# Performance work log

Hardware: AMD Instinct MI355X
Metric: run time of the kernel (lower is better)

## Reference

```python
import jax, jax.numpy as jnp
import numpy as np

B, S, D, H, FF = 16, 1024, 1024, 8, 4096
DH = D // H
EPS = 1e-5

def _ln(x, g, b):
    mu = jnp.mean(x, axis=-1, keepdims=True)
    var = jnp.mean((x - mu) ** 2, axis=-1, keepdims=True)
    return (x - mu) * jax.lax.rsqrt(var + EPS) * g + b

def setup_inputs() -> dict:
    key = jax.random.key(0)
    ks = jax.random.split(key, 12)
    sd = D ** -0.5
    return {
        "x": jax.random.normal(ks[0], (B, S, D), jnp.float32),
        "bias": jax.random.normal(ks[1], (S, S), jnp.float32),
        "Wq": jax.random.normal(ks[2], (D, D), jnp.float32) * sd,
        "bq": jnp.zeros((D,), jnp.float32),
        "Wk": jax.random.normal(ks[3], (D, D), jnp.float32) * sd,
        "bk": jnp.zeros((D,), jnp.float32),
        "Wv": jax.random.normal(ks[4], (D, D), jnp.float32) * sd,
        "bv": jnp.zeros((D,), jnp.float32),
        "Wo": jax.random.normal(ks[5], (D, D), jnp.float32) * sd,
        "bo": jnp.zeros((D,), jnp.float32),
        "ln1_g": jnp.ones((D,), jnp.float32),
        "ln1_b": jnp.zeros((D,), jnp.float32),
        "W1": jax.random.normal(ks[6], (FF, D), jnp.float32) * sd,
        "b1": jnp.zeros((FF,), jnp.float32),
        "W2": jax.random.normal(ks[7], (D, FF), jnp.float32) * (FF ** -0.5),
        "b2": jnp.zeros((D,), jnp.float32),
        "ln2_g": jnp.ones((D,), jnp.float32),
        "ln2_b": jnp.zeros((D,), jnp.float32),
    }

def reference(x, bias, Wq, bq, Wk, bk, Wv, bv, Wo, bo, ln1_g, ln1_b,
              W1, b1, W2, b2, ln2_g, ln2_b):
    # torch nn.Linear: y = x @ W.T + b
    Q = x @ Wq.T + bq  # [B,S,D]
    K = x @ Wk.T + bk
    V = x @ Wv.T + bv
    # Faithful to torch: plain row-major reshape [B,S,H*dh] -> [B*H,S,dh]
    Q = Q.reshape(B * H, S, DH)
    K = K.reshape(B * H, S, DH)
    V = V.reshape(B * H, S, DH)
    scale = DH ** -0.5
    scores = jnp.einsum('bqd,bkd->bqk', Q, K)  # [B*H,S,S]
    scores = (scores + bias[None]) * scale      # bias added BEFORE scaling, as in source
    attn = jax.nn.softmax(scores, axis=-1)
    selfattention = attn[0]
    ctx = jnp.einsum('bqk,bkd->bqd', attn, V).reshape(B, S, D)
    out = ctx @ Wo.T + bo
    out = _ln(out + x, ln1_g, ln1_b)
    # FFN
    h = jax.nn.relu(out @ W1.T + b1)
    ff = h @ W2.T + b2
    out2 = _ln(ff + out, ln2_g, ln2_b)
    return out2, selfattention
```

## Files before the change

### kernel.cpp

```cpp
#include <hip/hip_runtime.h>
#include <hip/hip_bf16.h>
#include <math.h>

typedef __attribute__((ext_vector_type(4))) float f32x4;
typedef __attribute__((ext_vector_type(8))) __bf16 bf16x8;
typedef __attribute__((ext_vector_type(4))) __bf16 bf16x4;

static constexpr float SCALE = 0.08838834764831845f;
static constexpr float SCALE_LOG2E = 0.1275174482f;

__device__ __forceinline__ void load_lds16(const void* g, void* l) {
  __builtin_amdgcn_global_load_lds(
      (const __attribute__((address_space(1))) void*)g,
      (__attribute__((address_space(3))) void*)l, 16, 0, 0);
}

__global__ __launch_bounds__(256) void cast_kernel(const float* __restrict__ s,
                                                   __bf16* __restrict__ d, int n4) {
  int i = blockIdx.x * blockDim.x + threadIdx.x;
  int stride = gridDim.x * blockDim.x;
  for (; i < n4; i += stride) {
    float4 v = reinterpret_cast<const float4*>(s)[i];
    bf16x4 o;
    o[0] = (__bf16)v.x; o[1] = (__bf16)v.y; o[2] = (__bf16)v.z; o[3] = (__bf16)v.w;
    reinterpret_cast<bf16x4*>(d)[i] = o;
  }
}

__global__ __launch_bounds__(256) void cast_weights(
    const float* __restrict__ wq, const float* __restrict__ wk,
    const float* __restrict__ wv, const float* __restrict__ wo,
    const float* __restrict__ w1, const float* __restrict__ w2,
    __bf16* __restrict__ dq, __bf16* __restrict__ dk,
    __bf16* __restrict__ dv, __bf16* __restrict__ dwo,
    __bf16* __restrict__ d1, __bf16* __restrict__ d2) {
  int i = blockIdx.x * blockDim.x + threadIdx.x;
  int stride = gridDim.x * blockDim.x;
  for (; i < 3145728; i += stride) {
    const float* s; __bf16* d; int j;
    if (i < 262144)       { s = wq; d = dq;  j = i; }
    else if (i < 524288)  { s = wk; d = dk;  j = i - 262144; }
    else if (i < 786432)  { s = wv; d = dv;  j = i - 524288; }
    else if (i < 1048576) { s = wo; d = dwo; j = i - 786432; }
    else if (i < 2097152) { s = w1; d = d1;  j = i - 1048576; }
    else                  { s = w2; d = d2;  j = i - 2097152; }
    float4 v = reinterpret_cast<const float4*>(s)[j];
    bf16x4 o;
    o[0] = (__bf16)v.x; o[1] = (__bf16)v.y; o[2] = (__bf16)v.z; o[3] = (__bf16)v.w;
    reinterpret_cast<bf16x4*>(d)[j] = o;
  }
}

__global__ __launch_bounds__(256) void scale_cast_kernel(const float* __restrict__ s,
                                                         __bf16* __restrict__ d, int n4) {
  int i = blockIdx.x * blockDim.x + threadIdx.x;
  int stride = gridDim.x * blockDim.x;
  for (; i < n4; i += stride) {
    float4 v = reinterpret_cast<const float4*>(s)[i];
    bf16x4 o;
    o[0] = (__bf16)(v.x * SCALE_LOG2E); o[1] = (__bf16)(v.y * SCALE_LOG2E);
    o[2] = (__bf16)(v.z * SCALE_LOG2E); o[3] = (__bf16)(v.w * SCALE_LOG2E);
    reinterpret_cast<bf16x4*>(d)[i] = o;
  }
}

template <int EPI>
__global__ __launch_bounds__(512, 2) void gemm_bt(
    const __bf16* __restrict__ A, const __bf16* __restrict__ Bw,
    const float* __restrict__ bvec, __bf16* __restrict__ Cb,
    float* __restrict__ Cf, int M, int N, int K) {
  __shared__ __align__(16) char sm[131072];

  const int ntn = N >> 8;
  const int nwg = gridDim.x;
  const int bid = blockIdx.x;
  const int b = (bid & 7) * (nwg >> 3) + (bid >> 3);
  const int tm = b / ntn, tn = b % ntn;
  const int t = threadIdx.x, lane = t & 63;
  const int w = t >> 6;
  const int wm = w >> 2, wn = w & 3;
  const int l15 = lane & 15, lq = lane >> 4;

  f32x4 acc[8][4] = {};

  const int r0 = t >> 3;
  const int r1 = r0 + 64;
  const int kb0 = (((t & 7) << 4) ^ ((r0 & 7) << 4));
  const int wbase = w << 10;

  auto stage = [&](int kt, int p) {
    char* base = sm + (p << 16);
    const size_t kofs = (size_t)(kb0 >> 1) + ((size_t)kt << 6);
#pragma unroll
    for (int h = 0; h < 2; ++h) {
      const __bf16* gA = A + (size_t)((tm << 8) + (h << 7) + r0) * K + kofs;
      const __bf16* gA2 = A + (size_t)((tm << 8) + (h << 7) + r1) * K + kofs;
      char* lA = base + (h << 14) + wbase;
      load_lds16(gA, lA);
      load_lds16(gA2, lA + 8192);
      const __bf16* gB = Bw + (size_t)((tn << 8) + (h << 7) + r0) * K + kofs;
      const __bf16* gB2 = Bw + (size_t)((tn << 8) + (h << 7) + r1) * K + kofs;
      char* lB = base + 32768 + (h << 14) + wbase;
      load_lds16(gB, lB);
      load_lds16(gB2, lB + 8192);
    }
  };

  stage(0, 0);
  __syncthreads();

  const int NT = K >> 6;
  const int rbB = (wn & 1) << 6;
  for (int kt = 0; kt < NT; ++kt) {
    const int p = kt & 1;
    const char* Ab = sm + (p << 16) + (wm << 14);
    const char* Bb = sm + (p << 16) + 32768 + ((wn >> 1) << 14);
    if (kt + 1 < NT) stage(kt + 1, p ^ 1);

    bf16x8 bfv[4][2];
#pragma unroll
    for (int nf = 0; nf < 4; ++nf) {
      const int r = rbB + (nf << 4) + l15;
      const int sw = (r & 7) << 4;
#pragma unroll
      for (int ks = 0; ks < 2; ++ks) {
        const int lb = (ks << 6) + (lq << 4);
        bfv[nf][ks] = *(const bf16x8*)(Bb + r * 128 + (lb ^ sw));
      }
    }
#pragma unroll
    for (int q = 0; q < 4; ++q) {
      bf16x8 af[2][2];
#pragma unroll
      for (int dm = 0; dm < 2; ++dm) {
        const int r = (((q << 1) + dm) << 4) + l15;
        const int sw = (r & 7) << 4;
#pragma unroll
        for (int ks = 0; ks < 2; ++ks) {
          const int lb = (ks << 6) + (lq << 4);
          af[dm][ks] = *(const bf16x8*)(Ab + r * 128 + (lb ^ sw));
        }
      }
#pragma unroll
      for (int ks = 0; ks < 2; ++ks)
#pragma unroll
        for (int dm = 0; dm < 2; ++dm)
#pragma unroll
          for (int nf = 0; nf < 4; ++nf)
            acc[(q << 1) + dm][nf] = __builtin_amdgcn_mfma_f32_16x16x32_bf16(
                af[dm][ks], bfv[nf][ks], acc[(q << 1) + dm][nf], 0, 0, 0);
    }
    __syncthreads();
  }

  const int row0 = (tm << 8) + (wm << 7) + (lq << 2);
  const int col0 = (tn << 8) + (wn << 6) + l15;
#pragma unroll
  for (int nf = 0; nf < 4; ++nf) {
    const int col = col0 + (nf << 4);
    const float bv = bvec[col];
#pragma unroll
    for (int mf = 0; mf < 8; ++mf) {
#pragma unroll
      for (int r = 0; r < 4; ++r) {
        const int row = row0 + (mf << 4) + r;
        float v = acc[mf][nf][r] + bv;
        if (EPI == 1) v = fmaxf(v, 0.f);
        if (EPI == 2) {
          Cf[(size_t)row * N + col] = v;
        } else if (EPI == 3) {
          size_t vt = ((size_t)(row >> 7) << 17) + ((size_t)(col & 127) << 10) +
                      ((row & 127) << 3) + (col >> 7);
          Cb[vt] = (__bf16)v;
        } else {
          Cb[(size_t)row * N + col] = (__bf16)v;
        }
      }
    }
  }
}

__global__ __launch_bounds__(512, 2) void gemm_qkv(
    const __bf16* __restrict__ A,
    const __bf16* __restrict__ Wq, const __bf16* __restrict__ Wk,
    const __bf16* __restrict__ Wv,
    const float* __restrict__ bqv, const float* __restrict__ bkv,
    const float* __restrict__ bvv,
    __bf16* __restrict__ Qo, __bf16* __restrict__ Ko, __bf16* __restrict__ VTo) {
  __shared__ __align__(16) char sm[131072];
  const int K = 1024, N = 1024;

  const int bid = blockIdx.x;
  const int b = (bid & 7) * 96 + (bid >> 3);
  const int tm = b / 12;
  const int tnt = b % 12;
  const int mi = tnt >> 2, tn = tnt & 3;
  const __bf16* Bw = (mi == 0) ? Wq : (mi == 1) ? Wk : Wv;
  const float* bvec = (mi == 0) ? bqv : (mi == 1) ? bkv : bvv;
  __bf16* Cb = (mi == 0) ? Qo : (mi == 1) ? Ko : VTo;

  const int t = threadIdx.x, lane = t & 63;
  const int w = t >> 6;
  const int wm = w >> 2, wn = w & 3;
  const int l15 = lane & 15, lq = lane >> 4;

  f32x4 acc[8][4] = {};

  const int r0 = t >> 3;
  const int r1 = r0 + 64;
  const int kb0 = (((t & 7) << 4) ^ ((r0 & 7) << 4));
  const int wbase = w << 10;

  auto stage = [&](int kt, int p) {
    char* base = sm + (p << 16);
    const size_t kofs = (size_t)(kb0 >> 1) + ((size_t)kt << 6);
#pragma unroll
    for (int h = 0; h < 2; ++h) {
      const __bf16* gA = A + (size_t)((tm << 8) + (h << 7) + r0) * K + kofs;
      const __bf16* gA2 = A + (size_t)((tm << 8) + (h << 7) + r1) * K + kofs;
      char* lA = base + (h << 14) + wbase;
      load_lds16(gA, lA);
      load_lds16(gA2, lA + 8192);
      const __bf16* gB = Bw + (size_t)((tn << 8) + (h << 7) + r0) * K + kofs;
      const __bf16* gB2 = Bw + (size_t)((tn << 8) + (h << 7) + r1) * K + kofs;
      char* lB = base + 32768 + (h << 14) + wbase;
      load_lds16(gB, lB);
      load_lds16(gB2, lB + 8192);
    }
  };

  stage(0, 0);
  __syncthreads();

  const int NT = K >> 6;
  const int rbB = (wn & 1) << 6;
  for (int kt = 0; kt < NT; ++kt) {
    const int p = kt & 1;
    const char* Ab = sm + (p << 16) + (wm << 14);
    const char* Bb = sm + (p << 16) + 32768 + ((wn >> 1) << 14);
    if (kt + 1 < NT) stage(kt + 1, p ^ 1);

    bf16x8 bfv[4][2];
#pragma unroll
    for (int nf = 0; nf < 4; ++nf) {
      const int r = rbB + (nf << 4) + l15;
      const int sw = (r & 7) << 4;
#pragma unroll
      for (int ks = 0; ks < 2; ++ks) {
        const int lb = (ks << 6) + (lq << 4);
        bfv[nf][ks] = *(const bf16x8*)(Bb + r * 128 + (lb ^ sw));
      }
    }
#pragma unroll
    for (int q = 0; q < 4; ++q) {
      bf16x8 af[2][2];
#pragma unroll
      for (int dm = 0; dm < 2; ++dm) {
        const int r = (((q << 1) + dm) << 4) + l15;
        const int sw = (r & 7) << 4;
#pragma unroll
        for (int ks = 0; ks < 2; ++ks) {
          const int lb = (ks << 6) + (lq << 4);
          af[dm][ks] = *(const bf16x8*)(Ab + r * 128 + (lb ^ sw));
        }
      }
#pragma unroll
      for (int ks = 0; ks < 2; ++ks)
#pragma unroll
        for (int dm = 0; dm < 2; ++dm)
#pragma unroll
          for (int nf = 0; nf < 4; ++nf)
            acc[(q << 1) + dm][nf] = __builtin_amdgcn_mfma_f32_16x16x32_bf16(
                af[dm][ks], bfv[nf][ks], acc[(q << 1) + dm][nf], 0, 0, 0);
    }
    __syncthreads();
  }

  const int row0 = (tm << 8) + (wm << 7) + (lq << 2);
  const int col0 = (tn << 8) + (wn << 6) + l15;
#pragma unroll
  for (int nf = 0; nf < 4; ++nf) {
    const int col = col0 + (nf << 4);
    const float bv = bvec[col];
#pragma unroll
    for (int mf = 0; mf < 8; ++mf) {
#pragma unroll
      for (int r = 0; r < 4; ++r) {
        const int row = row0 + (mf << 4) + r;
        float v = acc[mf][nf][r] + bv;
        if (mi == 2) {
          size_t vt = ((size_t)(row >> 7) << 17) + ((size_t)(col & 127) << 10) +
                      ((row & 127) << 3) + (col >> 7);
          Cb[vt] = (__bf16)v;
        } else {
          Cb[(size_t)row * N + col] = (__bf16)v;
        }
      }
    }
  }
}

__global__ __launch_bounds__(256) void attn_flash(
    const __bf16* __restrict__ Q, const __bf16* __restrict__ K,
    const __bf16* __restrict__ VT, const __bf16* __restrict__ biasS,
    __bf16* __restrict__ ctx) {
  __shared__ __bf16 Ks[64 * 128];
  __shared__ __bf16 VTs[128 * 64];
  __shared__ __bf16 Ps[4][16 * 64];

  const int bid = blockIdx.x;
  const int b = ((bid & 7) << 8) | (bid >> 3);
  const int g = b >> 4;
  const int q0 = (b & 15) << 6;
  const size_t goff = (size_t)g << 17;
  const __bf16* Qg = Q + goff;
  const __bf16* Kg = K + goff;
  const __bf16* VTg = VT + goff;

  const int t = threadIdx.x, w = t >> 6, lane = t & 63;
  const int l15 = lane & 15, lq = lane >> 4;
  const int qg = q0 + (w << 4) + l15;

  bf16x8 qf[4];
  {
    const __bf16* qrow = Qg + (size_t)qg * 128 + (lq << 3);
#pragma unroll
    for (int ec = 0; ec < 4; ++ec) qf[ec] = *(const bf16x8*)(qrow + (ec << 5));
  }
  const __bf16* bSr = biasS + ((size_t)qg << 10) + (lq << 2);

  float lrun = 0.f;
  f32x4 cacc[8] = {};

  for (int kb = 0; kb < 1024; kb += 64) {
    {
      int srow = lane >> 4;
      int sbo = (lane & 15) << 4;
#pragma unroll
      for (int i = 0; i < 4; ++i) {
        int c = (w << 2) + i;
        int r = (c << 2) + srow;
        int ke = (sbo ^ ((r & 7) << 4)) >> 1;
        load_lds16(Kg + (size_t)(kb + r) * 128 + ke, (char*)Ks + (c << 10));
      }
    }
    {
      int srow = lane >> 3;
      int sbo = (lane & 7) << 4;
#pragma unroll
      for (int i = 0; i < 4; ++i) {
        int c = (w << 2) + i;
        int e = (c << 3) + srow;
        int ke = kb + ((sbo ^ ((e & 7) << 4)) >> 1);
        load_lds16(VTg + (size_t)e * 1024 + ke, (char*)VTs + (c << 10));
      }
    }
    __syncthreads();

    f32x4 sacc[4] = {};
    __builtin_amdgcn_s_setprio(1);
#pragma unroll
    for (int ec = 0; ec < 4; ++ec) {
      const int lb = (ec << 6) + (lq << 4);
#pragma unroll
      for (int kn = 0; kn < 4; ++kn) {
        int rb = (kn << 4) + l15;
        bf16x8 kf = *(const bf16x8*)((const char*)Ks + rb * 256 + (lb ^ ((rb & 7) << 4)));
        sacc[kn] = __builtin_amdgcn_mfma_f32_16x16x32_bf16(kf, qf[ec], sacc[kn], 0, 0, 0);
      }
    }
    __builtin_amdgcn_s_setprio(0);

    const __bf16* bt = bSr + kb;
#pragma unroll
    for (int kn = 0; kn < 4; ++kn) {
      bf16x4 bb = *(const bf16x4*)(bt + (kn << 4));
      bf16x4 pk;
#pragma unroll
      for (int r = 0; r < 4; ++r) {
        float p = exp2f(fmaf(sacc[kn][r], SCALE_LOG2E, (float)bb[r]));
        lrun += p;
        pk[r] = (__bf16)p;
      }
      int bo = (kn << 5) + (lq << 3);
      *(bf16x4*)((char*)Ps[w] + l15 * 128 + (bo ^ ((l15 & 7) << 4))) = pk;
    }
    asm volatile("s_waitcnt lgkmcnt(0)" ::: "memory");
    __builtin_amdgcn_sched_barrier(0);

    __builtin_amdgcn_s_setprio(1);
#pragma unroll
    for (int ks = 0; ks < 2; ++ks) {
      const int lb = (ks << 6) + (lq << 4);
      bf16x8 paf = *(const bf16x8*)((const char*)Ps[w] + l15 * 128 + (lb ^ ((l15 & 7) << 4)));
#pragma unroll
      for (int et = 0; et < 8; ++et) {
        int e = (et << 4) + l15;
        bf16x8 vf = *(const bf16x8*)((const char*)VTs + e * 128 + (lb ^ ((e & 7) << 4)));
        cacc[et] = __builtin_amdgcn_mfma_f32_16x16x32_bf16(paf, vf, cacc[et], 0, 0, 0);
      }
    }
    __builtin_amdgcn_s_setprio(0);
    __syncthreads();
  }

  lrun += __shfl_xor(lrun, 16);
  lrun += __shfl_xor(lrun, 32);
  float lrunR[4];
#pragma unroll
  for (int r = 0; r < 4; ++r)
    lrunR[r] = __shfl(lrun, (lane & 48) + ((lane & 48) >> 2) + r);
  __bf16* cg = ctx + goff;
  const int qr = q0 + (w << 4) + (lq << 2);
#pragma unroll
  for (int et = 0; et < 8; ++et)
#pragma unroll
    for (int r = 0; r < 4; ++r) {
      float v = cacc[et][r] / lrunR[r];
      cg[(size_t)(qr + r) * 128 + (et << 4) + l15] = (__bf16)v;
    }
}

__global__ __launch_bounds__(256) void attn_head0(
    const __bf16* __restrict__ Q, const __bf16* __restrict__ K,
    const float* __restrict__ bias, float* __restrict__ out) {
  __shared__ float qrow[128];
  __shared__ float red[8];
  const int q = blockIdx.x, t = threadIdx.x;
  if (t < 128) qrow[t] = (float)Q[(size_t)q * 128 + t];
  __syncthreads();
  float s[4];
#pragma unroll
  for (int c = 0; c < 4; ++c) {
    int kc = (c << 8) + t;
    const __bf16* kr = K + (size_t)kc * 128;
    float dot = 0.f;
#pragma unroll
    for (int e = 0; e < 128; e += 8) {
      bf16x8 kv = *(const bf16x8*)(kr + e);
#pragma unroll
      for (int j = 0; j < 8; ++j) dot += qrow[e + j] * (float)kv[j];
    }
    s[c] = (dot + bias[(size_t)q * 1024 + kc]) * SCALE;
  }
  float mx = fmaxf(fmaxf(s[0], s[1]), fmaxf(s[2], s[3]));
#pragma unroll
  for (int d = 32; d >= 1; d >>= 1) mx = fmaxf(mx, __shfl_xor(mx, d));
  const int w = t >> 6, lane = t & 63;
  if (lane == 0) red[w] = mx;
  __syncthreads();
  mx = fmaxf(fmaxf(red[0], red[1]), fmaxf(red[2], red[3]));
  float ex[4], sum = 0.f;
#pragma unroll
  for (int c = 0; c < 4; ++c) { ex[c] = __expf(s[c] - mx); sum += ex[c]; }
#pragma unroll
  for (int d = 32; d >= 1; d >>= 1) sum += __shfl_xor(sum, d);
  __syncthreads();
  if (lane == 0) red[4 + w] = sum;
  __syncthreads();
  sum = red[4] + red[5] + red[6] + red[7];
  float inv = 1.f / sum;
#pragma unroll
  for (int c = 0; c < 4; ++c) out[(size_t)q * 1024 + (c << 8) + t] = ex[c] * inv;
}

template <int A_BF16, int B_BF16>
__global__ __launch_bounds__(256) void ln_res(
    const void* __restrict__ aptr, const void* __restrict__ bptr,
    const float* __restrict__ gam, const float* __restrict__ bet,
    float* __restrict__ outf, __bf16* __restrict__ outb) {
  __shared__ float red[8];
  const int row = blockIdx.x, t = threadIdx.x;
  const size_t base = (size_t)row << 10;
  float a0, a1, a2, a3;
  if (A_BF16) {
    bf16x4 va = reinterpret_cast<const bf16x4*>((const __bf16*)aptr + base)[t];
    a0 = (float)va[0]; a1 = (float)va[1]; a2 = (float)va[2]; a3 = (float)va[3];
  } else {
    float4 va = reinterpret_cast<const float4*>((const float*)aptr + base)[t];
    a0 = va.x; a1 = va.y; a2 = va.z; a3 = va.w;
  }
  float b0, b1, b2, b3;
  if (B_BF16) {
    bf16x4 vb = reinterpret_cast<const bf16x4*>((const __bf16*)bptr + base)[t];
    b0 = (float)vb[0]; b1 = (float)vb[1]; b2 = (float)vb[2]; b3 = (float)vb[3];
  } else {
    float4 vb = reinterpret_cast<const float4*>((const float*)bptr + base)[t];
    b0 = vb.x; b1 = vb.y; b2 = vb.z; b3 = vb.w;
  }
  float v0 = a0 + b0, v1 = a1 + b1, v2 = a2 + b2, v3 = a3 + b3;
  float s = v0 + v1 + v2 + v3;
  float qq = v0 * v0 + v1 * v1 + v2 * v2 + v3 * v3;
#pragma unroll
  for (int d = 32; d >= 1; d >>= 1) {
    s += __shfl_xor(s, d);
    qq += __shfl_xor(qq, d);
  }
  const int w = t >> 6, lane = t & 63;
  if (lane == 0) { red[w] = s; red[4 + w] = qq; }
  __syncthreads();
  s = red[0] + red[1] + red[2] + red[3];
  qq = red[4] + red[5] + red[6] + red[7];
  const float mu = s * (1.f / 1024.f);
  const float var = qq * (1.f / 1024.f) - mu * mu;
  const float rs = rsqrtf(var + 1e-5f);
  float4 g4 = reinterpret_cast<const float4*>(gam)[t];
  float4 b4 = reinterpret_cast<const float4*>(bet)[t];
  float o0 = (v0 - mu) * rs * g4.x + b4.x;
  float o1 = (v1 - mu) * rs * g4.y + b4.y;
  float o2 = (v2 - mu) * rs * g4.z + b4.z;
  float o3 = (v3 - mu) * rs * g4.w + b4.w;
  if (outf) reinterpret_cast<float4*>(outf + base)[t] = make_float4(o0, o1, o2, o3);
  if (outb) {
    bf16x4 ob;
    ob[0] = (__bf16)o0; ob[1] = (__bf16)o1; ob[2] = (__bf16)o2; ob[3] = (__bf16)o3;
    reinterpret_cast<bf16x4*>(outb + base)[t] = ob;
  }
}

extern "C" void kernel_launch(void* const* d_in, const int* in_sizes, int n_in,
                              void* d_out, int out_size, void* d_ws, size_t ws_size,
                              hipStream_t stream) {
  (void)in_sizes; (void)n_in; (void)out_size; (void)ws_size;
  const float* x    = (const float*)d_in[0];
  const float* bias = (const float*)d_in[1];
  const float* Wq   = (const float*)d_in[2];
  const float* bq   = (const float*)d_in[3];
  const float* Wk   = (const float*)d_in[4];
  const float* bk   = (const float*)d_in[5];
  const float* Wv   = (const float*)d_in[6];
  const float* bv   = (const float*)d_in[7];
  const float* Wo   = (const float*)d_in[8];
  const float* bo   = (const float*)d_in[9];
  const float* g1   = (const float*)d_in[10];
  const float* b1l  = (const float*)d_in[11];
  const float* W1   = (const float*)d_in[12];
  const float* b1f  = (const float*)d_in[13];
  const float* W2   = (const float*)d_in[14];
  const float* b2f  = (const float*)d_in[15];
  const float* g2   = (const float*)d_in[16];
  const float* b2l  = (const float*)d_in[17];

  char* ws = (char*)d_ws;
  size_t off = 0;
  auto alloc = [&](size_t bytes) {
    char* p = ws + off;
    off += (bytes + 255) & ~(size_t)255;
    return p;
  };
  __bf16* wqb  = (__bf16*)alloc(2097152);
  __bf16* wkb  = (__bf16*)alloc(2097152);
  __bf16* wvb  = (__bf16*)alloc(2097152);
  __bf16* wob  = (__bf16*)alloc(2097152);
  __bf16* w1b  = (__bf16*)alloc(8388608);
  __bf16* w2b  = (__bf16*)alloc(8388608);
  __bf16* biasS = (__bf16*)alloc(2097152);
  __bf16* xb   = (__bf16*)alloc(33554432);
  __bf16* Qb   = (__bf16*)alloc(4ull * 33554432);
  __bf16* Kb   = Qb + 16777216;
  __bf16* VTb  = Kb + 16777216;
  __bf16* ctxb = VTb + 16777216;
  __bf16* hb   = Qb;
  __bf16* res1b = xb;
  __bf16* attn_out_b = Qb;

  float* out2     = (float*)d_out;
  float* selfattn = (float*)d_out + 16777216;
  float* ff       = out2;

  cast_kernel<<<2048, 256, 0, stream>>>(x, xb, 16777216 / 4);
  cast_weights<<<2048, 256, 0, stream>>>(Wq, Wk, Wv, Wo, W1, W2,
                                         wqb, wkb, wvb, wob, w1b, w2b);
  scale_cast_kernel<<<512, 256, 0, stream>>>(bias, biasS, 1048576 / 4);

  gemm_qkv<<<768, 512, 0, stream>>>(xb, wqb, wkb, wvb, bq, bk, bv, Qb, Kb, VTb);

  attn_head0<<<1024, 256, 0, stream>>>(Qb, Kb, bias, selfattn);
  attn_flash<<<128 * 16, 256, 0, stream>>>(Qb, Kb, VTb, biasS, ctxb);

  gemm_bt<0><<<64 * 4, 512, 0, stream>>>(ctxb, wob, bo, attn_out_b, nullptr, 16384, 1024, 1024);

  ln_res<1, 0><<<16384, 256, 0, stream>>>(attn_out_b, x, g1, b1l, nullptr, res1b);

  gemm_bt<1><<<64 * 16, 512, 0, stream>>>(res1b, w1b, b1f, hb, nullptr, 16384, 4096, 1024);
  gemm_bt<2><<<64 * 4, 512, 0, stream>>>(hb, w2b, b2f, nullptr, ff, 16384, 1024, 4096);

  ln_res<0, 1><<<16384, 256, 0, stream>>>(ff, res1b, g2, b2l, out2, nullptr);
}
```

Baseline: 747.8 us.

## Add phased-barrier FFN GEMM, widen attention blocks, split QKV GEMM

Adds a templated GEMM (gemm_ph) for the two FFN GEMMs. It issues the next tile's global-to-LDS load after the first sub-step and uses raw s_barrier/waitcnt plus setprio around each MFMA group, so copies overlap compute with finer sync. The fused QKV GEMM is replaced by three gemm_bt launches, the V launch using the transposed epilogue. The flash attention kernel now runs 8 waves per block over 128 query rows, so each staged K/V tile is reused by twice as many rows. The first LayerNorm reads the bf16 copy of x as its residual instead of fp32, which cuts traffic but lowers residual precision.

```diff
diff --git a/kernel.cpp b/kernel.cpp
--- a/kernel.cpp
+++ b/kernel.cpp
@@ -180,25 +180,18 @@
   }
 }
 
-__global__ __launch_bounds__(512, 2) void gemm_qkv(
-    const __bf16* __restrict__ A,
-    const __bf16* __restrict__ Wq, const __bf16* __restrict__ Wk,
-    const __bf16* __restrict__ Wv,
-    const float* __restrict__ bqv, const float* __restrict__ bkv,
-    const float* __restrict__ bvv,
-    __bf16* __restrict__ Qo, __bf16* __restrict__ Ko, __bf16* __restrict__ VTo) {
+template <int EPI>
+__global__ __launch_bounds__(512, 2) void gemm_ph(
+    const __bf16* __restrict__ A, const __bf16* __restrict__ Bw,
+    const float* __restrict__ bvec, __bf16* __restrict__ Cb,
+    float* __restrict__ Cf, int M, int N, int K) {
   __shared__ __align__(16) char sm[131072];
-  const int K = 1024, N = 1024;
-
+
+  const int ntn = N >> 8;
+  const int nwg = gridDim.x;
   const int bid = blockIdx.x;
-  const int b = (bid & 7) * 96 + (bid >> 3);
-  const int tm = b / 12;
-  const int tnt = b % 12;
-  const int mi = tnt >> 2, tn = tnt & 3;
-  const __bf16* Bw = (mi == 0) ? Wq : (mi == 1) ? Wk : Wv;
-  const float* bvec = (mi == 0) ? bqv : (mi == 1) ? bkv : bvv;
-  __bf16* Cb = (mi == 0) ? Qo : (mi == 1) ? Ko : VTo;
-
+  const int b = (bid & 7) * (nwg >> 3) + (bid >> 3);
+  const int tm = b / ntn, tn = b % ntn;
   const int t = threadIdx.x, lane = t & 63;
   const int w = t >> 6;
   const int wm = w >> 2, wn = w & 3;
@@ -230,7 +223,7 @@
   };
 
   stage(0, 0);
-  __syncthreads();
+  asm volatile("s_waitcnt vmcnt(0)\ns_barrier" ::: "memory");
 
   const int NT = K >> 6;
   const int rbB = (wn & 1) << 6;
@@ -238,7 +231,6 @@
     const int p = kt & 1;
     const char* Ab = sm + (p << 16) + (wm << 14);
     const char* Bb = sm + (p << 16) + 32768 + ((wn >> 1) << 14);
-    if (kt + 1 < NT) stage(kt + 1, p ^ 1);
 
     bf16x8 bfv[4][2];
 #pragma unroll
@@ -251,6 +243,7 @@
         bfv[nf][ks] = *(const bf16x8*)(Bb + r * 128 + (lb ^ sw));
       }
     }
+
 #pragma unroll
     for (int q = 0; q < 4; ++q) {
       bf16x8 af[2][2];
@@ -264,6 +257,11 @@
           af[dm][ks] = *(const bf16x8*)(Ab + r * 128 + (lb ^ sw));
         }
       }
+      if (q == 0 && kt + 1 < NT) stage(kt + 1, p ^ 1);
+      asm volatile("s_barrier" ::: "memory");
+      asm volatile("s_waitcnt lgkmcnt(0)" ::: "memory");
+      __builtin_amdgcn_sched_barrier(0);
+      __builtin_amdgcn_s_setprio(1);
 #pragma unroll
       for (int ks = 0; ks < 2; ++ks)
 #pragma unroll
@@ -272,8 +270,10 @@
           for (int nf = 0; nf < 4; ++nf)
             acc[(q << 1) + dm][nf] = __builtin_amdgcn_mfma_f32_16x16x32_bf16(
                 af[dm][ks], bfv[nf][ks], acc[(q << 1) + dm][nf], 0, 0, 0);
-    }
-    __syncthreads();
+      __builtin_amdgcn_s_setprio(0);
+      if (q == 3) asm volatile("s_waitcnt vmcnt(0)" ::: "memory");
+      asm volatile("s_barrier" ::: "memory");
+    }
   }
 
   const int row0 = (tm << 8) + (wm << 7) + (lq << 2);
@@ -288,30 +288,28 @@
       for (int r = 0; r < 4; ++r) {
         const int row = row0 + (mf << 4) + r;
         float v = acc[mf][nf][r] + bv;
-        if (mi == 2) {
-          size_t vt = ((size_t)(row >> 7) << 17) + ((size_t)(col & 127) << 10) +
-                      ((row & 127) << 3) + (col >> 7);
-          Cb[vt] = (__bf16)v;
-        } else {
+        if (EPI == 1) v = fmaxf(v, 0.f);
+        if (EPI == 2)
+          Cf[(size_t)row * N + col] = v;
+        else
           Cb[(size_t)row * N + col] = (__bf16)v;
-        }
-      }
-    }
-  }
-}
-
-__global__ __launch_bounds__(256) void attn_flash(
+      }
+    }
+  }
+}
+
+__global__ __launch_bounds__(512, 2) void attn_flash(
     const __bf16* __restrict__ Q, const __bf16* __restrict__ K,
     const __bf16* __restrict__ VT, const __bf16* __restrict__ biasS,
     __bf16* __restrict__ ctx) {
   __shared__ __bf16 Ks[64 * 128];
   __shared__ __bf16 VTs[128 * 64];
-  __shared__ __bf16 Ps[4][16 * 64];
+  __shared__ __bf16 Ps[8][16 * 64];
 
   const int bid = blockIdx.x;
-  const int b = ((bid & 7) << 8) | (bid >> 3);
-  const int g = b >> 4;
-  const int q0 = (b & 15) << 6;
+  const int b = ((bid & 7) << 7) | (bid >> 3);
+  const int g = b >> 3;
+  const int q0 = (b & 7) << 7;
   const size_t goff = (size_t)g << 17;
   const __bf16* Qg = Q + goff;
   const __bf16* Kg = K + goff;
@@ -337,8 +335,8 @@
       int srow = lane >> 4;
       int sbo = (lane & 15) << 4;
 #pragma unroll
-      for (int i = 0; i < 4; ++i) {
-        int c = (w << 2) + i;
+      for (int i = 0; i < 2; ++i) {
+        int c = (w << 1) + i;
         int r = (c << 2) + srow;
         int ke = (sbo ^ ((r & 7) << 4)) >> 1;
         load_lds16(Kg + (size_t)(kb + r) * 128 + ke, (char*)Ks + (c << 10));
@@ -348,8 +346,8 @@
       int srow = lane >> 3;
       int sbo = (lane & 7) << 4;
 #pragma unroll
-      for (int i = 0; i < 4; ++i) {
-        int c = (w << 2) + i;
+      for (int i = 0; i < 2; ++i) {
+        int c = (w << 1) + i;
         int e = (c << 3) + srow;
         int ke = kb + ((sbo ^ ((e & 7) << 4)) >> 1);
         load_lds16(VTg + (size_t)e * 1024 + ke, (char*)VTs + (c << 10));
@@ -573,17 +571,19 @@
                                          wqb, wkb, wvb, wob, w1b, w2b);
   scale_cast_kernel<<<512, 256, 0, stream>>>(bias, biasS, 1048576 / 4);
 
-  gemm_qkv<<<768, 512, 0, stream>>>(xb, wqb, wkb, wvb, bq, bk, bv, Qb, Kb, VTb);
+  gemm_bt<0><<<64 * 4, 512, 0, stream>>>(xb, wqb, bq, Qb, nullptr, 16384, 1024, 1024);
+  gemm_bt<0><<<64 * 4, 512, 0, stream>>>(xb, wkb, bk, Kb, nullptr, 16384, 1024, 1024);
+  gemm_bt<3><<<64 * 4, 512, 0, stream>>>(xb, wvb, bv, VTb, nullptr, 16384, 1024, 1024);
 
   attn_head0<<<1024, 256, 0, stream>>>(Qb, Kb, bias, selfattn);
-  attn_flash<<<128 * 16, 256, 0, stream>>>(Qb, Kb, VTb, biasS, ctxb);
+  attn_flash<<<128 * 8, 512, 0, stream>>>(Qb, Kb, VTb, biasS, ctxb);
 
   gemm_bt<0><<<64 * 4, 512, 0, stream>>>(ctxb, wob, bo, attn_out_b, nullptr, 16384, 1024, 1024);
 
-  ln_res<1, 0><<<16384, 256, 0, stream>>>(attn_out_b, x, g1, b1l, nullptr, res1b);
-
-  gemm_bt<1><<<64 * 16, 512, 0, stream>>>(res1b, w1b, b1f, hb, nullptr, 16384, 4096, 1024);
-  gemm_bt<2><<<64 * 4, 512, 0, stream>>>(hb, w2b, b2f, nullptr, ff, 16384, 1024, 4096);
+  ln_res<1, 1><<<16384, 256, 0, stream>>>(attn_out_b, xb, g1, b1l, nullptr, res1b);
+
+  gemm_ph<1><<<64 * 16, 512, 0, stream>>>(res1b, w1b, b1f, hb, nullptr, 16384, 4096, 1024);
+  gemm_ph<2><<<64 * 4, 512, 0, stream>>>(hb, w2b, b2f, nullptr, ff, 16384, 1024, 4096);
 
   ln_res<0, 1><<<16384, 256, 0, stream>>>(ff, res1b, g2, b2l, out2, nullptr);
 }
```

Measured after the change: 743.3 us. No clear change (-0.6%).
